# Kernel tuning notes

Hardware: AMD Instinct MI355X
Metric: run time of the kernel (lower is better)

The kernel has to match this reference:

```python
import jax, jax.numpy as jnp
import numpy as np

B, S, D, H = 8, 1024, 768, 12
HD = D // H  # head_dim = 64


def setup_inputs() -> dict:
    key = jax.random.key(0)
    ks = jax.random.split(key, 9)
    s = 0.02
    return {
        "hidden_states": jax.random.normal(ks[0], (B, S, D), dtype=jnp.float32),
        "Wq": jax.random.normal(ks[1], (D, D), dtype=jnp.float32) * s,
        "bq": jnp.zeros((D,), dtype=jnp.float32),
        "Wk": jax.random.normal(ks[2], (D, D), dtype=jnp.float32) * s,
        "bk": jnp.zeros((D,), dtype=jnp.float32),
        "Wv": jax.random.normal(ks[3], (D, D), dtype=jnp.float32) * s,
        "bv": jnp.zeros((D,), dtype=jnp.float32),
        "Wo": jax.random.normal(ks[4], (D, D), dtype=jnp.float32) * s,
        "bo": jnp.zeros((D,), dtype=jnp.float32),
    }


def reference(hidden_states, Wq, bq, Wk, bk, Wv, bv, Wo, bo):
    b, s, d = hidden_states.shape
    scale = 1.0 / jnp.sqrt(jnp.asarray(HD, dtype=hidden_states.dtype))
    # projections (weights stored as [in, out])
    q = hidden_states @ Wq + bq
    k = hidden_states @ Wk + bk
    v = hidden_states @ Wv + bv
    # [B, H, S, HD]
    q = q.reshape(b, s, H, HD).transpose(0, 2, 1, 3)
    k = k.reshape(b, s, H, HD).transpose(0, 2, 1, 3)
    v = v.reshape(b, s, H, HD).transpose(0, 2, 1, 3)
    # explicit O(S^2) attention, matching the original unfused math
    attn = jnp.einsum("bhqd,bhkd->bhqk", q, k) * scale
    attn = jax.nn.softmax(attn, axis=-1)
    out = jnp.einsum("bhqk,bhkd->bhqd", attn, v)
    out = out.transpose(0, 2, 1, 3).reshape(b, s, d)
    return out @ Wo + bo
```

## Files before the change

### kernel.cpp

```cpp
#include <hip/hip_runtime.h>
#include <stdint.h>

#define DEV __device__ __forceinline__

typedef __attribute__((ext_vector_type(8))) short bf16x8;
typedef __attribute__((ext_vector_type(4))) float f32x4;

#define MFMA16(a,b,c) __builtin_amdgcn_mfma_f32_16x16x32_bf16((a),(b),(c),0,0,0)

#define GL_LDS(SRC, DST) \
  __builtin_amdgcn_global_load_lds( \
      (const __attribute__((address_space(1))) void*)(SRC), \
      (__attribute__((address_space(3))) void*)(DST), 16, 0, 0)

DEV unsigned short f2bf(float x){
  union { float f; unsigned u; } v; v.f = x;
  unsigned r = v.u + 0x7fffu + ((v.u >> 16) & 1u);
  return (unsigned short)(r >> 16);
}
DEV unsigned pack2(float a, float b){
  return (unsigned)f2bf(a) | ((unsigned)f2bf(b) << 16);
}
DEV unsigned pack2_rtz(float a, float b){
  union { float f; unsigned u; } ua, ub; ua.f = a; ub.f = b;
  return (ua.u >> 16) | (ub.u & 0xffff0000u);
}
DEV bf16x8 mk_bf16x8(unsigned w0, unsigned w1, unsigned w2, unsigned w3){
  union { uint4 u; bf16x8 v; } cv;
  cv.u = make_uint4(w0, w1, w2, w3);
  return cv.v;
}
DEV void bar(){
  asm volatile("" ::: "memory");
  __builtin_amdgcn_s_barrier();
  asm volatile("" ::: "memory");
}

__global__ void cast_x_kernel(const float* __restrict__ x, uint4* __restrict__ out){
  int i = blockIdx.x * 256 + threadIdx.x;
  const float4* p = (const float4*)x + (size_t)i * 2;
  float4 a = p[0], b = p[1];
  out[i] = make_uint4(pack2(a.x,a.y), pack2(a.z,a.w), pack2(b.x,b.y), pack2(b.z,b.w));
}

__global__ void trans_w_kernel(const float* __restrict__ W0, const float* __restrict__ W1,
                               const float* __restrict__ W2, const float* __restrict__ W3,
                               unsigned short* __restrict__ T0, unsigned short* __restrict__ T1,
                               unsigned short* __restrict__ T2, unsigned short* __restrict__ T3){
  const float* W; unsigned short* T;
  switch (blockIdx.z) {
    case 0:  W = W0; T = T0; break;
    case 1:  W = W1; T = T1; break;
    case 2:  W = W2; T = T2; break;
    default: W = W3; T = T3; break;
  }
  __shared__ float tile[32][33];
  const int i0 = blockIdx.y * 32, o0 = blockIdx.x * 32;
  const int t = threadIdx.x;
  const int ir = t >> 3, oc = (t & 7) * 4;
  float4 v = *(const float4*)(W + (size_t)(i0 + ir) * 768 + o0 + oc);
  tile[ir][oc+0] = v.x; tile[ir][oc+1] = v.y; tile[ir][oc+2] = v.z; tile[ir][oc+3] = v.w;
  __syncthreads();
  const int orow = t >> 3, ic = (t & 7) * 4;
  uint2 w;
  w.x = pack2(tile[ic+0][orow], tile[ic+1][orow]);
  w.y = pack2(tile[ic+2][orow], tile[ic+3][orow]);
  *(uint2*)(T + (size_t)(o0 + orow) * 768 + i0 + ic) = w;
}

__launch_bounds__(512, 2)
__global__ void gemm_qkv(const unsigned short* __restrict__ Wcat,
                         const unsigned short* __restrict__ X16,
                         const float* __restrict__ bq, const float* __restrict__ bk,
                         const float* __restrict__ bv,
                         unsigned short* __restrict__ Qb, unsigned short* __restrict__ Kb,
                         unsigned short* __restrict__ VTb)
{
  __shared__ __align__(16) unsigned char a_lds[2][2][18432];
  __shared__ __align__(16) unsigned char b_lds[2][2][16384];
  const int tid = threadIdx.x;
  const int lane = tid & 63;
  const int wid = tid >> 6;
  const int lin = blockIdx.x;
  const int nid = (lin & 7) * 32 + (lin >> 3);
  const int m0 = (nid & 7) * 288;
  const int n0 = (nid >> 3) * 256;
  const int wm = wid >> 2, wn = wid & 3;

  const int c1 = tid,               r1 = ((c1 >> 6) << 4) + (c1 & 15), kg1 = (c1 >> 4) & 3;
  const int c2 = 512 + tid,         r2 = ((c2 >> 6) << 4) + (c2 & 15), kg2 = (c2 >> 4) & 3;
  const int c3 = 1024 + (tid & 127),r3 = ((c3 >> 6) << 4) + (c3 & 15), kg3 = (c3 >> 4) & 3;
  const unsigned short* Abase = Wcat + (size_t)m0 * 768;
  const unsigned short* Bbase = X16  + (size_t)n0 * 768;

  #define STAGE_A(TILE, KK) do {                                                   \
    const int ko_ = (TILE) * 64 + (KK) * 32;                                       \
    GL_LDS(Abase + (size_t)r1 * 768 + ko_ + kg1 * 8, &a_lds[(TILE)&1][KK][c1*16]); \
    GL_LDS(Abase + (size_t)r2 * 768 + ko_ + kg2 * 8, &a_lds[(TILE)&1][KK][c2*16]); \
    GL_LDS(Abase + (size_t)r3 * 768 + ko_ + kg3 * 8, &a_lds[(TILE)&1][KK][c3*16]); \
  } while (0)
  #define STAGE_B(TILE, KK) do {                                                   \
    const int ko_ = (TILE) * 64 + (KK) * 32;                                       \
    GL_LDS(Bbase + (size_t)r1 * 768 + ko_ + kg1 * 8, &b_lds[(TILE)&1][KK][c1*16]); \
    GL_LDS(Bbase + (size_t)r2 * 768 + ko_ + kg2 * 8, &b_lds[(TILE)&1][KK][c2*16]); \
  } while (0)

  #define PHASE(BUF, KK, STAGE_STMT)                                               \
  {                                                                                \
    bf16x8 b0 = *(const bf16x8*)&b_lds[BUF][KK][((wn*4+0)*64+lane)*16];            \
    bf16x8 b1 = *(const bf16x8*)&b_lds[BUF][KK][((wn*4+1)*64+lane)*16];            \
    STAGE_STMT;                                                                    \
    bar();                                                                         \
    __builtin_amdgcn_s_setprio(1);                                                 \
    _Pragma("unroll")                                                              \
    for (int mb = 0; mb < 9; ++mb) {                                               \
      bf16x8 af = *(const bf16x8*)&a_lds[BUF][KK][((wm*9+mb)*64+lane)*16];         \
      acc[mb][0] = MFMA16(af, b0, acc[mb][0]);                                     \
      acc[mb][1] = MFMA16(af, b1, acc[mb][1]);                                     \
    }                                                                              \
    bf16x8 b2 = *(const bf16x8*)&b_lds[BUF][KK][((wn*4+2)*64+lane)*16];            \
    bf16x8 b3 = *(const bf16x8*)&b_lds[BUF][KK][((wn*4+3)*64+lane)*16];            \
    _Pragma("unroll")                                                              \
    for (int mb = 0; mb < 9; ++mb) {                                               \
      bf16x8 af = *(const bf16x8*)&a_lds[BUF][KK][((wm*9+mb)*64+lane)*16];         \
      acc[mb][2] = MFMA16(af, b2, acc[mb][2]);                                     \
      acc[mb][3] = MFMA16(af, b3, acc[mb][3]);                                     \
    }                                                                              \
    __builtin_amdgcn_s_setprio(0);                                                 \
    asm volatile("s_waitcnt vmcnt(10)" ::: "memory");                              \
    bar();                                                                         \
  }

  f32x4 acc[9][4] = {};

  STAGE_A(0, 0);
  STAGE_B(0, 0);
  STAGE_A(0, 1);
  STAGE_B(0, 1);
  STAGE_A(1, 0);
  STAGE_B(1, 0);
  asm volatile("s_waitcnt vmcnt(10)" ::: "memory");
  bar();

  for (int i = 0; i < 6; ++i) {
    const int k0t = 2 * i, k1t = 2 * i + 1;
    const bool pf = (i < 5);
    PHASE(0, 0, { STAGE_A(k1t, 1);     STAGE_B(k1t, 1);     })
    PHASE(0, 1, { if (pf) { STAGE_A(k0t + 2, 0); STAGE_B(k0t + 2, 0); } })
    PHASE(1, 0, { if (pf) { STAGE_A(k0t + 2, 1); STAGE_B(k0t + 2, 1); } })
    PHASE(1, 1, { if (pf) { STAGE_A(k1t + 2, 0); STAGE_B(k1t + 2, 0); } })
  }
  #undef PHASE
  #undef STAGE_A
  #undef STAGE_B

  const int l15 = lane & 15, lg = lane >> 4;
  #pragma unroll
  for (int mb = 0; mb < 9; ++mb) {
    const int chan_g = m0 + wm * 144 + mb * 16 + lg * 4;
    const int sel  = chan_g / 768;
    const int chan = chan_g - sel * 768;
    const int h = chan >> 6, hd = chan & 63;
    #pragma unroll
    for (int nb = 0; nb < 4; ++nb) {
      const int coll = wn * 64 + nb * 16 + l15;
      const int sg   = n0 + coll;
      const int b = sg >> 10, s = sg & 1023;
      f32x4 a = acc[mb][nb];
      if (sel != 2) {
        float4 bi = *(const float4*)((sel == 0 ? bq : bk) + chan);
        uint2 w;
        w.x = pack2(a[0] + bi.x, a[1] + bi.y);
        w.y = pack2(a[2] + bi.z, a[3] + bi.w);
        unsigned short* o = (sel == 0 ? Qb : Kb);
        *(uint2*)(o + ((size_t)(b * 12 + h) * 1024 + s) * 64 + hd) = w;
      } else {
        float4 bi = *(const float4*)(bv + chan);
        size_t base = ((size_t)(b * 12 + h) * 64 + hd) * 1024 + s;
        VTb[base       ] = f2bf(a[0] + bi.x);
        VTb[base + 1024] = f2bf(a[1] + bi.y);
        VTb[base + 2048] = f2bf(a[2] + bi.z);
        VTb[base + 3072] = f2bf(a[3] + bi.w);
      }
    }
  }
}

__launch_bounds__(256, 3)
__global__ void gemm_out(const unsigned short* __restrict__ matA,
                         const unsigned short* __restrict__ matB,
                         float* __restrict__ outp,
                         const float* __restrict__ bias)
{
  __shared__ __align__(16) unsigned char ldsA[2][4096];
  __shared__ __align__(16) unsigned char ldsB[2][8192];
  const int lane = threadIdx.x & 63, wid = threadIdx.x >> 6;
  const int lin = blockIdx.x;
  const int nid = (lin & 7) * 96 + (lin >> 3);
  const int m0 = (nid % 12) * 64;
  const int n0 = (nid / 12) * 128;
  const int wm = wid >> 1, wn = wid & 1;

  f32x4 acc[2][4] = {};

  for (int t = 0; t < 24; ++t) {
    const int buf = t & 1;
    const int k0 = t * 32;
    {
      const int c   = wid * 64 + lane;
      const int row = ((c >> 6) << 4) + (c & 15);
      const int kk  = ((c >> 4) & 3) * 8;
      const unsigned short* sa = matA + (size_t)(m0 + row) * 768 + k0 + kk;
      GL_LDS(sa, &ldsA[buf][c * 16]);
    }
    #pragma unroll
    for (int i = 0; i < 2; ++i) {
      const int c   = i * 256 + wid * 64 + lane;
      const int row = ((c >> 6) << 4) + (c & 15);
      const int kk  = ((c >> 4) & 3) * 8;
      const unsigned short* sb = matB + (size_t)(n0 + row) * 768 + k0 + kk;
      GL_LDS(sb, &ldsB[buf][c * 16]);
    }
    __syncthreads();

    bf16x8 afr[2], bfr[4];
    #pragma unroll
    for (int mb = 0; mb < 2; ++mb)
      afr[mb] = *(const bf16x8*)&ldsA[buf][((wm * 2 + mb) * 64 + lane) * 16];
    #pragma unroll
    for (int nb = 0; nb < 4; ++nb)
      bfr[nb] = *(const bf16x8*)&ldsB[buf][((wn * 4 + nb) * 64 + lane) * 16];
    #pragma unroll
    for (int mb = 0; mb < 2; ++mb)
      #pragma unroll
      for (int nb = 0; nb < 4; ++nb)
        acc[mb][nb] = MFMA16(afr[mb], bfr[nb], acc[mb][nb]);
  }

  const int l15 = lane & 15, lg = lane >> 4;
  #pragma unroll
  for (int mb = 0; mb < 2; ++mb) {
    #pragma unroll
    for (int nb = 0; nb < 4; ++nb) {
      const int rowl = wm * 32 + mb * 16 + lg * 4;
      const int coll = wn * 64 + nb * 16 + l15;
      f32x4 a = acc[mb][nb];
      int chan = m0 + rowl, sg = n0 + coll;
      float4 bi = *(const float4*)(bias + chan);
      float4 o = make_float4(a[0] + bi.x, a[1] + bi.y, a[2] + bi.z, a[3] + bi.w);
      *(float4*)(outp + (size_t)sg * 768 + chan) = o;
    }
  }
}

__launch_bounds__(256, 4)
__global__ void attn_kernel(const unsigned short* __restrict__ Q,
                            const unsigned short* __restrict__ K,
                            const unsigned short* __restrict__ VT,
                            unsigned short* __restrict__ AO)
{
  __shared__ __align__(16) unsigned char kbuf[8192];
  __shared__ __align__(16) unsigned char vbuf[8192];
  const int lane = threadIdx.x & 63, wid = threadIdx.x >> 6;
  const int l15 = lane & 15, lg = lane >> 4;
  const int bh = blockIdx.x;
  const int q0 = blockIdx.y * 128 + wid * 32;
  const unsigned short* Qp = Q  + (size_t)bh * 65536;
  const unsigned short* Kp = K  + (size_t)bh * 65536;
  const unsigned short* Vp = VT + (size_t)bh * 65536;

  bf16x8 qf[2][2];
  #pragma unroll
  for (int f = 0; f < 2; ++f)
    #pragma unroll
    for (int kc = 0; kc < 2; ++kc)
      qf[f][kc] = *(const bf16x8*)(Qp + (size_t)(q0 + f * 16 + l15) * 64 + kc * 32 + lg * 8);

  f32x4 acco[2][4] = {};
  float lsum[2] = {0.f, 0.f};

  const int src0 = l15 + ((lg & 1) << 5);
  const int src1 = src0 + 16;
  const bool hi = (lg & 2) != 0;

  for (int t = 0; t < 16; ++t) {
    const int kv0 = t * 64;
    #pragma unroll
    for (int i = 0; i < 2; ++i) {
      const int g = wid * 2 + i;
      const unsigned short* sk = Kp + (size_t)(kv0 + (g >> 1) * 16 + l15) * 64 + (g & 1) * 32 + lg * 8;
      GL_LDS(sk, &kbuf[g * 1024]);
      const unsigned short* sv = Vp + (size_t)((g >> 1) * 16 + l15) * 1024 + kv0 + (g & 1) * 32 + lg * 8;
      GL_LDS(sv, &vbuf[g * 1024]);
    }
    __syncthreads();

    f32x4 sc[2][4] = {};
    __builtin_amdgcn_s_setprio(1);
    #pragma unroll
    for (int mb = 0; mb < 4; ++mb) {
      #pragma unroll
      for (int kc = 0; kc < 2; ++kc) {
        bf16x8 kf = *(const bf16x8*)&kbuf[((mb * 2 + kc) * 64 + lane) * 16];
        sc[0][mb] = MFMA16(kf, qf[0][kc], sc[0][mb]);
        sc[1][mb] = MFMA16(kf, qf[1][kc], sc[1][mb]);
      }
    }
    __builtin_amdgcn_s_setprio(0);
    unsigned p01[2][4], p23[2][4];
    #pragma unroll
    for (int f = 0; f < 2; ++f) {
      float sum = 0.f;
      #pragma unroll
      for (int mb = 0; mb < 4; ++mb) {
        float e0 = __expf(sc[f][mb][0] * 0.125f);
        float e1 = __expf(sc[f][mb][1] * 0.125f);
        float e2 = __expf(sc[f][mb][2] * 0.125f);
        float e3 = __expf(sc[f][mb][3] * 0.125f);
        sum += (e0 + e1) + (e2 + e3);
        p01[f][mb] = pack2_rtz(e0, e1);
        p23[f][mb] = pack2_rtz(e2, e3);
      }
      sum += __shfl_xor(sum, 16);
      sum += __shfl_xor(sum, 32);
      lsum[f] += sum;
    }
    bf16x8 pf[2][2];
    #pragma unroll
    for (int f = 0; f < 2; ++f) {
      #pragma unroll
      for (int c = 0; c < 2; ++c) {
        unsigned a0 = __shfl(p01[f][2*c], src0), b0 = __shfl(p01[f][2*c+1], src0);
        unsigned a1 = __shfl(p23[f][2*c], src0), b1 = __shfl(p23[f][2*c+1], src0);
        unsigned a2 = __shfl(p01[f][2*c], src1), b2 = __shfl(p01[f][2*c+1], src1);
        unsigned a3 = __shfl(p23[f][2*c], src1), b3 = __shfl(p23[f][2*c+1], src1);
        pf[f][c] = mk_bf16x8(hi ? b0 : a0, hi ? b1 : a1, hi ? b2 : a2, hi ? b3 : a3);
      }
    }
    __builtin_amdgcn_s_setprio(1);
    #pragma unroll
    for (int hb = 0; hb < 4; ++hb) {
      #pragma unroll
      for (int c = 0; c < 2; ++c) {
        bf16x8 vf = *(const bf16x8*)&vbuf[((hb * 2 + c) * 64 + lane) * 16];
        acco[0][hb] = MFMA16(vf, pf[0][c], acco[0][hb]);
        acco[1][hb] = MFMA16(vf, pf[1][c], acco[1][hb]);
      }
    }
    __builtin_amdgcn_s_setprio(0);
    __syncthreads();
  }

  const int b = bh / 12, h = bh % 12;
  #pragma unroll
  for (int f = 0; f < 2; ++f) {
    const float rl = 1.0f / lsum[f];
    const int s = q0 + f * 16 + l15;
    const size_t base = ((size_t)(b * 1024 + s)) * 768 + h * 64;
    #pragma unroll
    for (int hb = 0; hb < 4; ++hb) {
      uint2 w;
      w.x = pack2_rtz(acco[f][hb][0] * rl, acco[f][hb][1] * rl);
      w.y = pack2_rtz(acco[f][hb][2] * rl, acco[f][hb][3] * rl);
      *(uint2*)(AO + base + hb * 16 + lg * 4) = w;
    }
  }
}

extern "C" void kernel_launch(void* const* d_in, const int* in_sizes, int n_in,
                              void* d_out, int out_size, void* d_ws, size_t ws_size,
                              hipStream_t stream)
{
  const float* hs = (const float*)d_in[0];
  const float* Wq = (const float*)d_in[1];
  const float* bq = (const float*)d_in[2];
  const float* Wk = (const float*)d_in[3];
  const float* bk = (const float*)d_in[4];
  const float* Wv = (const float*)d_in[5];
  const float* bv = (const float*)d_in[6];
  const float* Wo = (const float*)d_in[7];
  const float* bo = (const float*)d_in[8];

  const size_t SZ_X = (size_t)8192 * 768 * 2;
  const size_t SZ_W = (size_t)768 * 768 * 2;
  const size_t NEED = SZ_X * 5 + SZ_W * 4;
  if (ws_size < NEED) return;

  char* ws = (char*)d_ws;
  unsigned short* X16 = (unsigned short*)ws;
  unsigned short* Wqt = (unsigned short*)(ws + SZ_X);
  unsigned short* Wkt = Wqt + 768 * 768;
  unsigned short* Wvt = Wkt + 768 * 768;
  unsigned short* Wot = Wvt + 768 * 768;
  unsigned short* Qb  = (unsigned short*)(ws + SZ_X + 4 * SZ_W);
  unsigned short* Kb  = Qb  + (size_t)8192 * 768;
  unsigned short* VTb = Kb  + (size_t)8192 * 768;
  unsigned short* AOb = VTb + (size_t)8192 * 768;

  cast_x_kernel<<<dim3(3072), dim3(256), 0, stream>>>(hs, (uint4*)X16);
  trans_w_kernel<<<dim3(24, 24, 4), dim3(256), 0, stream>>>(Wq, Wk, Wv, Wo, Wqt, Wkt, Wvt, Wot);

  gemm_qkv<<<dim3(256), dim3(512), 0, stream>>>(Wqt, X16, bq, bk, bv, Qb, Kb, VTb);

  attn_kernel<<<dim3(96, 8), dim3(256), 0, stream>>>(Qb, Kb, VTb, AOb);

  gemm_out<<<dim3(768), dim3(256), 0, stream>>>(Wot, AOb, (float*)d_out, bo);
}
```

Measured before the change: 141.0 us.

## Halve QKV GEMM N-tile and simplify to single-stage K32 double buffering

The QKV projection GEMM tile shrinks from 288x256 to 288x128, which doubles the grid to 512 blocks and raises launch bounds to 4 blocks per CU. The four-phase K=64 pipeline is replaced by a simpler loop over K=32 steps with a two-buffer prefetch. The aim is more resident blocks and better CU coverage with less LDS per block. In exchange each block gets less operand reuse, there are more barriers per unit of work, and the pipeline is shallower.

```diff
diff --git a/kernel.cpp b/kernel.cpp
--- a/kernel.cpp
+++ b/kernel.cpp
@@ -68,7 +68,7 @@
   *(uint2*)(T + (size_t)(o0 + orow) * 768 + i0 + ic) = w;
 }
 
-__launch_bounds__(512, 2)
+__launch_bounds__(512, 4)
 __global__ void gemm_qkv(const unsigned short* __restrict__ Wcat,
                          const unsigned short* __restrict__ X16,
                          const float* __restrict__ bq, const float* __restrict__ bk,
@@ -76,83 +76,58 @@
                          unsigned short* __restrict__ Qb, unsigned short* __restrict__ Kb,
                          unsigned short* __restrict__ VTb)
 {
-  __shared__ __align__(16) unsigned char a_lds[2][2][18432];
-  __shared__ __align__(16) unsigned char b_lds[2][2][16384];
+  __shared__ __align__(16) unsigned char a_lds[2][18432];
+  __shared__ __align__(16) unsigned char b_lds[2][8192];
   const int tid = threadIdx.x;
   const int lane = tid & 63;
   const int wid = tid >> 6;
   const int lin = blockIdx.x;
-  const int nid = (lin & 7) * 32 + (lin >> 3);
-  const int m0 = (nid & 7) * 288;
-  const int n0 = (nid >> 3) * 256;
+  const int nid = (lin & 7) * 64 + (lin >> 3);
+  const int m0 = (nid >> 6) * 288;
+  const int n0 = (nid & 63) * 128;
   const int wm = wid >> 2, wn = wid & 3;
 
-  const int c1 = tid,               r1 = ((c1 >> 6) << 4) + (c1 & 15), kg1 = (c1 >> 4) & 3;
-  const int c2 = 512 + tid,         r2 = ((c2 >> 6) << 4) + (c2 & 15), kg2 = (c2 >> 4) & 3;
-  const int c3 = 1024 + (tid & 127),r3 = ((c3 >> 6) << 4) + (c3 & 15), kg3 = (c3 >> 4) & 3;
+  const int c1 = tid,                r1 = ((c1 >> 6) << 4) + (c1 & 15), kg1 = (c1 >> 4) & 3;
+  const int c2 = 512 + tid,          r2 = ((c2 >> 6) << 4) + (c2 & 15), kg2 = (c2 >> 4) & 3;
+  const int c3 = 1024 + (tid & 127), r3 = ((c3 >> 6) << 4) + (c3 & 15), kg3 = (c3 >> 4) & 3;
   const unsigned short* Abase = Wcat + (size_t)m0 * 768;
   const unsigned short* Bbase = X16  + (size_t)n0 * 768;
 
-  #define STAGE_A(TILE, KK) do {                                                   \
-    const int ko_ = (TILE) * 64 + (KK) * 32;                                       \
-    GL_LDS(Abase + (size_t)r1 * 768 + ko_ + kg1 * 8, &a_lds[(TILE)&1][KK][c1*16]); \
-    GL_LDS(Abase + (size_t)r2 * 768 + ko_ + kg2 * 8, &a_lds[(TILE)&1][KK][c2*16]); \
-    GL_LDS(Abase + (size_t)r3 * 768 + ko_ + kg3 * 8, &a_lds[(TILE)&1][KK][c3*16]); \
+  #define STAGE(TILE) do {                                                        \
+    const int ko_ = (TILE) * 32;                                                  \
+    GL_LDS(Abase + (size_t)r1 * 768 + ko_ + kg1 * 8, &a_lds[(TILE)&1][c1*16]);    \
+    GL_LDS(Abase + (size_t)r2 * 768 + ko_ + kg2 * 8, &a_lds[(TILE)&1][c2*16]);    \
+    GL_LDS(Abase + (size_t)r3 * 768 + ko_ + kg3 * 8, &a_lds[(TILE)&1][c3*16]);    \
+    GL_LDS(Bbase + (size_t)r1 * 768 + ko_ + kg1 * 8, &b_lds[(TILE)&1][c1*16]);    \
   } while (0)
-  #define STAGE_B(TILE, KK) do {                                                   \
-    const int ko_ = (TILE) * 64 + (KK) * 32;                                       \
-    GL_LDS(Bbase + (size_t)r1 * 768 + ko_ + kg1 * 8, &b_lds[(TILE)&1][KK][c1*16]); \
-    GL_LDS(Bbase + (size_t)r2 * 768 + ko_ + kg2 * 8, &b_lds[(TILE)&1][KK][c2*16]); \
-  } while (0)
-
-  #define PHASE(BUF, KK, STAGE_STMT)                                               \
-  {                                                                                \
-    bf16x8 b0 = *(const bf16x8*)&b_lds[BUF][KK][((wn*4+0)*64+lane)*16];            \
-    bf16x8 b1 = *(const bf16x8*)&b_lds[BUF][KK][((wn*4+1)*64+lane)*16];            \
-    STAGE_STMT;                                                                    \
-    bar();                                                                         \
-    __builtin_amdgcn_s_setprio(1);                                                 \
-    _Pragma("unroll")                                                              \
-    for (int mb = 0; mb < 9; ++mb) {                                               \
-      bf16x8 af = *(const bf16x8*)&a_lds[BUF][KK][((wm*9+mb)*64+lane)*16];         \
-      acc[mb][0] = MFMA16(af, b0, acc[mb][0]);                                     \
-      acc[mb][1] = MFMA16(af, b1, acc[mb][1]);                                     \
-    }                                                                              \
-    bf16x8 b2 = *(const bf16x8*)&b_lds[BUF][KK][((wn*4+2)*64+lane)*16];            \
-    bf16x8 b3 = *(const bf16x8*)&b_lds[BUF][KK][((wn*4+3)*64+lane)*16];            \
-    _Pragma("unroll")                                                              \
-    for (int mb = 0; mb < 9; ++mb) {                                               \
-      bf16x8 af = *(const bf16x8*)&a_lds[BUF][KK][((wm*9+mb)*64+lane)*16];         \
-      acc[mb][2] = MFMA16(af, b2, acc[mb][2]);                                     \
-      acc[mb][3] = MFMA16(af, b3, acc[mb][3]);                                     \
-    }                                                                              \
-    __builtin_amdgcn_s_setprio(0);                                                 \
-    asm volatile("s_waitcnt vmcnt(10)" ::: "memory");                              \
-    bar();                                                                         \
-  }
-
-  f32x4 acc[9][4] = {};
-
-  STAGE_A(0, 0);
-  STAGE_B(0, 0);
-  STAGE_A(0, 1);
-  STAGE_B(0, 1);
-  STAGE_A(1, 0);
-  STAGE_B(1, 0);
-  asm volatile("s_waitcnt vmcnt(10)" ::: "memory");
-  bar();
-
-  for (int i = 0; i < 6; ++i) {
-    const int k0t = 2 * i, k1t = 2 * i + 1;
-    const bool pf = (i < 5);
-    PHASE(0, 0, { STAGE_A(k1t, 1);     STAGE_B(k1t, 1);     })
-    PHASE(0, 1, { if (pf) { STAGE_A(k0t + 2, 0); STAGE_B(k0t + 2, 0); } })
-    PHASE(1, 0, { if (pf) { STAGE_A(k0t + 2, 1); STAGE_B(k0t + 2, 1); } })
-    PHASE(1, 1, { if (pf) { STAGE_A(k1t + 2, 0); STAGE_B(k1t + 2, 0); } })
-  }
-  #undef PHASE
-  #undef STAGE_A
-  #undef STAGE_B
+
+  f32x4 acc[9][2] = {};
+
+  STAGE(0);
+
+  for (int t = 0; t < 24; ++t) {
+    const int buf = t & 1;
+    if (t < 23) {
+      STAGE(t + 1);
+      asm volatile("s_waitcnt vmcnt(4)" ::: "memory");
+    } else {
+      asm volatile("s_waitcnt vmcnt(0)" ::: "memory");
+    }
+    bar();
+
+    bf16x8 b0 = *(const bf16x8*)&b_lds[buf][((wn * 2 + 0) * 64 + lane) * 16];
+    bf16x8 b1 = *(const bf16x8*)&b_lds[buf][((wn * 2 + 1) * 64 + lane) * 16];
+    __builtin_amdgcn_s_setprio(1);
+    #pragma unroll
+    for (int mb = 0; mb < 9; ++mb) {
+      bf16x8 af = *(const bf16x8*)&a_lds[buf][((wm * 9 + mb) * 64 + lane) * 16];
+      acc[mb][0] = MFMA16(af, b0, acc[mb][0]);
+      acc[mb][1] = MFMA16(af, b1, acc[mb][1]);
+    }
+    __builtin_amdgcn_s_setprio(0);
+    bar();
+  }
+  #undef STAGE
 
   const int l15 = lane & 15, lg = lane >> 4;
   #pragma unroll
@@ -162,8 +137,8 @@
     const int chan = chan_g - sel * 768;
     const int h = chan >> 6, hd = chan & 63;
     #pragma unroll
-    for (int nb = 0; nb < 4; ++nb) {
-      const int coll = wn * 64 + nb * 16 + l15;
+    for (int nb = 0; nb < 2; ++nb) {
+      const int coll = wn * 32 + nb * 16 + l15;
       const int sg   = n0 + coll;
       const int b = sg >> 10, s = sg & 1023;
       f32x4 a = acc[mb][nb];
@@ -400,7 +375,7 @@
   cast_x_kernel<<<dim3(3072), dim3(256), 0, stream>>>(hs, (uint4*)X16);
   trans_w_kernel<<<dim3(24, 24, 4), dim3(256), 0, stream>>>(Wq, Wk, Wv, Wo, Wqt, Wkt, Wvt, Wot);
 
-  gemm_qkv<<<dim3(256), dim3(512), 0, stream>>>(Wqt, X16, bq, bk, bv, Qb, Kb, VTb);
+  gemm_qkv<<<dim3(512), dim3(512), 0, stream>>>(Wqt, X16, bq, bk, bv, Qb, Kb, VTb);
 
   attn_kernel<<<dim3(96, 8), dim3(256), 0, stream>>>(Qb, Kb, VTb, AOb);
 
```

After: 148.7 us. 5.5% more time.
